# Performance work log

Measured on AMD Instinct MI355X. Metric: run time of the kernel, lower is better.

The kernel has to match this reference:

```python
import jax, jax.numpy as jnp
import numpy as np

N_NODES = 50000
N_EDGES = 800000
NUM_GRAPHS = 256
H = 128          # h_dim
C = H + 1        # CGConv channels = 129
Z = 2 * C + 1    # concat(x_i, x_j, edge_attr) = 259
N_GRAPH_LAYERS = 5
N_FC = 3
OUT_DIM = 1


def setup_inputs() -> dict:
    key = jax.random.key(0)
    ks = jax.random.split(key, 12)
    atoms = jax.random.randint(ks[0], (N_NODES,), 0, 119)
    pos = jax.random.normal(ks[1], (N_NODES, 3), dtype=jnp.float32)
    edge_index = jax.random.randint(ks[2], (2, N_EDGES), 0, N_NODES)
    batch = jnp.sort(jax.random.randint(ks[3], (N_NODES,), 0, NUM_GRAPHS))
    s = 0.05
    emb = jax.random.normal(ks[4], (119, H), dtype=jnp.float32)
    Wf = jax.random.normal(ks[5], (N_GRAPH_LAYERS, Z, C), dtype=jnp.float32) * s
    bf = jnp.zeros((N_GRAPH_LAYERS, C), dtype=jnp.float32)
    Ws = jax.random.normal(ks[6], (N_GRAPH_LAYERS, Z, C), dtype=jnp.float32) * s
    bs = jnp.zeros((N_GRAPH_LAYERS, C), dtype=jnp.float32)
    Wfc = jax.random.normal(ks[7], (N_FC, C, C), dtype=jnp.float32) * s
    bfc = jnp.zeros((N_FC, C), dtype=jnp.float32)
    Wout = jax.random.normal(ks[8], (C, OUT_DIM), dtype=jnp.float32) * s
    bout = jnp.zeros((OUT_DIM,), dtype=jnp.float32)
    return {"atoms": atoms, "pos": pos, "edge_index": edge_index, "batch": batch,
            "emb": emb, "Wf": Wf, "bf": bf, "Ws": Ws, "bs": bs,
            "Wfc": Wfc, "bfc": bfc, "Wout": Wout, "bout": bout}


def reference(atoms, pos, edge_index, batch, emb, Wf, bf, Ws, bs, Wfc, bfc, Wout, bout):
    n = atoms.shape[0]
    src, dst = edge_index[0], edge_index[1]  # PyG: x_j = x[src], x_i = x[dst], aggregate at dst
    # edge_attr = ||pos[src] - pos[dst]||, shape [E, 1]
    edge_attr = jnp.linalg.norm(pos[src] - pos[dst], axis=-1, keepdims=True)
    # node features: atom embedding + z-coordinate -> [N, 129]
    x = jnp.concatenate([emb[atoms], pos[:, 2:3]], axis=-1)
    for l in range(Wf.shape[0]):
        z = jnp.concatenate([x[dst], x[src], edge_attr], axis=-1)  # [E, 259]
        m = jax.nn.sigmoid(z @ Wf[l] + bf[l]) * jax.nn.softplus(z @ Ws[l] + bs[l])
        x = x + jax.ops.segment_sum(m, dst, num_segments=n)  # CGConv: aggr='add' + residual
    # mean pooling per graph
    sums = jax.ops.segment_sum(x, batch, num_segments=NUM_GRAPHS)
    cnts = jax.ops.segment_sum(jnp.ones((n, 1), x.dtype), batch, num_segments=NUM_GRAPHS)
    g = sums / jnp.maximum(cnts, 1.0)
    for l in range(Wfc.shape[0]):
        g = g @ Wfc[l] + bfc[l]
    return g @ Wout + bout
```

## Files before the change

kernel.cpp:

```cpp
#include <hip/hip_runtime.h>
#include <math.h>

#define N_NODES 50000
#define N_EDGES 800000
#define NUM_GRAPHS 256
#define NPADROWS 50048
#define CAP 64
#define SCLN -1.44269504088896f
#define SCLP 1.44269504088896f
#define C693 0.69314718056f
#define LROW 264

typedef __attribute__((ext_vector_type(8))) short short8;
typedef __attribute__((ext_vector_type(4))) float f32x4;
typedef __attribute__((ext_vector_type(2))) float f32x2;

__device__ __forceinline__ float fast_rcp(float x) {
#if __has_builtin(__builtin_amdgcn_rcpf)
  return __builtin_amdgcn_rcpf(x);
#else
  return 1.0f / x;
#endif
}
__device__ __forceinline__ float EX2(float x) {
#if __has_builtin(__builtin_amdgcn_exp2f)
  return __builtin_amdgcn_exp2f(x);
#else
  return exp2f(x);
#endif
}
__device__ __forceinline__ float LG2(float x) {
#if __has_builtin(__builtin_amdgcn_logf)
  return __builtin_amdgcn_logf(x);
#else
  return log2f(x);
#endif
}
__device__ __forceinline__ unsigned f2bf(float x) {
  unsigned u = __float_as_uint(x);
  return (u + 0x7fffu + ((u >> 16) & 1u)) >> 16;
}
__device__ __forceinline__ unsigned short bfr(float v) {
  return (unsigned short)((__float_as_uint(v) + 0x8000u) >> 16);
}
__device__ __forceinline__ unsigned pkbfr(float lo, float hi) {
  unsigned a = (__float_as_uint(lo) + 0x8000u) >> 16;
  unsigned b = (__float_as_uint(hi) + 0x8000u) & 0xffff0000u;
  return a | b;
}
__device__ __forceinline__ float u2f(unsigned u) { return __uint_as_float(u); }
__device__ __forceinline__ f32x2 mk2(float a, float b) {
  f32x2 r; r.x = a; r.y = b; return r;
}
__device__ __forceinline__ f32x2 unp(unsigned u) {
  return mk2(u2f(u << 16), u2f(u & 0xffff0000u));
}
__device__ __forceinline__ f32x2 lg2p1(f32x2 t) {
  f32x2 p = __builtin_elementwise_fma(t, (f32x2)0.0439245f, (f32x2)-0.1898214f);
  p = __builtin_elementwise_fma(t, p, (f32x2)0.4115517f);
  p = __builtin_elementwise_fma(t, p, (f32x2)-0.7072504f);
  p = __builtin_elementwise_fma(t, p, (f32x2)1.4415927f);
  return t * p;
}
__device__ __forceinline__ void edge_ch2(f32x2 gf, f32x2 gs, f32x2& acc) {
  f32x2 den = mk2(EX2(gf.x), EX2(gf.y)) + 1.0f;
  f32x2 ts = mk2(EX2(-fabsf(gs.x)), EX2(-fabsf(gs.y)));
  f32x2 sp = lg2p1(ts) + __builtin_elementwise_max(gs, (f32x2)0.0f);
  f32x2 rc = mk2(fast_rcp(den.x), fast_rcp(den.y));
  acc = __builtin_elementwise_fma(rc, sp, acc);
}

__global__ void init_x(const int* __restrict__ atoms, const float* __restrict__ pos,
                       const float* __restrict__ emb, float* __restrict__ x128c,
                       unsigned* __restrict__ xbu, float4* __restrict__ pos4,
                       int* __restrict__ cnt) {
  int n = blockIdx.x;
  int t = threadIdx.x;
  int a = atoms[n];
  float2 e = *(const float2*)(emb + (size_t)a * 128 + 2 * t);
  xbu[(size_t)n * 64 + t] = f2bf(e.x) | (f2bf(e.y) << 16);
  if (t == 0) x128c[n] = pos[n * 3 + 2];
  if (t == 1) pos4[n] = make_float4(pos[3 * n], pos[3 * n + 1], pos[3 * n + 2], 0.f);
  if (t == 2) cnt[n] = 0;
}

__global__ void prep_b(const float* __restrict__ Wf, const float* __restrict__ Ws,
                       const float* __restrict__ bfp, const float* __restrict__ bsp,
                       uint4* __restrict__ Bp, float2* __restrict__ Wtail) {
  int idx = blockIdx.x * 256 + threadIdx.x;
  if (idx < 5 * 4 * 9 * 4 * 64) {
    int lane = idx & 63;
    int t = idx >> 6;
    int ks = t & 3; t >>= 2;
    int ct = t % 9; t /= 9;
    int g = t & 3;
    int l = t >> 2;
    const float* W = (g >= 2) ? Ws : Wf;
    float sc = (g < 2) ? SCLN : SCLP;
    int col = ct * 16 + (lane & 15);
    int kb = ks * 32 + (lane >> 4) * 8;
    unsigned u[4];
#pragma unroll
    for (int p = 0; p < 4; ++p) {
      unsigned lo = 0, hi = 0;
      if (col < 129) {
        int k0 = kb + 2 * p, k1 = k0 + 1;
        int r0 = (g & 1) ? 129 + k0 : k0;
        int r1 = (g & 1) ? 129 + k1 : k1;
        lo = f2bf(sc * W[(size_t)(l * 259 + r0) * 129 + col]);
        hi = f2bf(sc * W[(size_t)(l * 259 + r1) * 129 + col]);
      }
      u[p] = lo | (hi << 16);
    }
    Bp[idx] = make_uint4(u[0], u[1], u[2], u[3]);
  } else {
    int j = idx - 5 * 4 * 9 * 4 * 64;
    if (j >= 5 * 4 * 144) return;
    int c = j % 144;
    int t = j / 144;
    int g = t & 3;
    int l = t >> 2;
    float sc = (g < 2) ? SCLN : SCLP;
    float w1 = 0.0f, bias = 0.0f;
    if (c <= 128) {
      const float* W = (g >= 2) ? Ws : Wf;
      int row = (g & 1) ? 257 : 128;
      w1 = sc * W[(size_t)(l * 259 + row) * 129 + c];
      if (g == 0) bias = SCLN * bfp[l * 129 + c];
      if (g == 2) bias = SCLP * bsp[l * 129 + c];
    }
    Wtail[(l * 4 + g) * 144 + c] = make_float2(w1, bias);
  }
}

__global__ void build_csr(const int* __restrict__ ei, const float4* __restrict__ pos4,
                          const int* __restrict__ batch, int* __restrict__ cnt,
                          int2* __restrict__ csr, int* __restrict__ goff) {
  int e = blockIdx.x * 256 + threadIdx.x;
  if (e <= N_NODES) {
    int b = (e < N_NODES) ? batch[e] : NUM_GRAPHS;
    int bp = (e > 0) ? batch[e - 1] : -1;
    for (int g = bp + 1; g <= b; ++g) goff[g] = e;
  }
  if (e >= N_EDGES) return;
  int s = ei[e];
  int d = ei[N_EDGES + e];
  float4 ps = pos4[s];
  float4 pd = pos4[d];
  float dx = ps.x - pd.x, dy = ps.y - pd.y, dz = ps.z - pd.z;
  float ea = sqrtf(dx * dx + dy * dy + dz * dz);
  int p = atomicAdd(&cnt[d], 1);
  if (p < CAP) csr[d * CAP + p] = make_int2(s, __float_as_int(ea));
}

__global__ __launch_bounds__(256) void gemm_mfma(
    const unsigned* __restrict__ xbu, const float* __restrict__ x128c,
    const uint4* __restrict__ Bp, const float2* __restrict__ Wtail,
    unsigned short* __restrict__ Pdh, unsigned short* __restrict__ Pfs,
    unsigned* __restrict__ Pd128c, unsigned* __restrict__ Pc128, int layer) {
  __shared__ short smA[32 * 136];
  __shared__ unsigned short ldsD[32 * LROW];
  __shared__ unsigned short ldsS[32 * LROW];
  int n0 = blockIdx.x * 32;
  int tid = threadIdx.x;
  for (int ch = tid; ch < 512; ch += 256) {
    int row = ch >> 4, cq = ch & 15;
    *(uint4*)(&smA[row * 136 + cq * 8]) =
        *(const uint4*)(xbu + (size_t)(n0 + row) * 64 + cq * 4);
  }
  __syncthreads();
  int g = tid >> 6;
  int l = tid & 63;
  int q = l >> 4, c16 = l & 15;
  const short8* Bp8 = (const short8*)Bp;
  int bbase = (layer * 4 + g) * 9 * 4;
  f32x4 acc[2][9];
#pragma unroll
  for (int rt = 0; rt < 2; ++rt)
#pragma unroll
    for (int ct = 0; ct < 9; ++ct) acc[rt][ct] = (f32x4){0.f, 0.f, 0.f, 0.f};
#pragma unroll
  for (int ks = 0; ks < 4; ++ks) {
    short8 a0 = *(const short8*)(&smA[c16 * 136 + (ks * 4 + q) * 8]);
    short8 a1 = *(const short8*)(&smA[(16 + c16) * 136 + (ks * 4 + q) * 8]);
#pragma unroll
    for (int ct = 0; ct < 9; ++ct) {
      short8 b = Bp8[(size_t)(bbase + ct * 4 + ks) * 64 + l];
      acc[0][ct] = __builtin_amdgcn_mfma_f32_16x16x32_bf16(a0, b, acc[0][ct], 0, 0, 0);
      acc[1][ct] = __builtin_amdgcn_mfma_f32_16x16x32_bf16(a1, b, acc[1][ct], 0, 0, 0);
    }
  }
  const float2* Wt = Wtail + (layer * 4 + g) * 144;
  float x128[2][4];
#pragma unroll
  for (int rt = 0; rt < 2; ++rt)
#pragma unroll
    for (int r = 0; r < 4; ++r)
      x128[rt][r] = x128c[n0 + rt * 16 + q * 4 + r];
  unsigned short* ldsO = (g & 1) ? ldsS : ldsD;
  int soff = (g >= 2) ? 2 : 0;
  unsigned short* c128p = (g & 1) ? (unsigned short*)Pc128 : (unsigned short*)Pd128c;
  int c128o = (g >= 2) ? 1 : 0;
#pragma unroll
  for (int ct = 0; ct < 9; ++ct) {
    int col = ct * 16 + c16;
    float2 wb = Wt[col];
#pragma unroll
    for (int rt = 0; rt < 2; ++rt) {
#pragma unroll
      for (int r = 0; r < 4; ++r) {
        int rl = rt * 16 + q * 4 + r;
        float v = acc[rt][ct][r] + fmaf(x128[rt][r], wb.x, wb.y);
        if (col < 128) {
          ldsO[rl * LROW + ((col >> 1) << 2) + soff + (col & 1)] = bfr(v);
        } else if (col == 128) {
          c128p[2 * (size_t)(n0 + rl) + c128o] = bfr(v);
        }
      }
    }
  }
  __syncthreads();
#pragma unroll
  for (int i = tid; i < 2048; i += 256) {
    int img = i >> 10;
    int c = i & 1023;
    int row = c >> 5, part = c & 31;
    const unsigned short* src = (img ? ldsS : ldsD) + row * LROW + part * 8;
    unsigned short* dst = (img ? Pfs : Pdh) + (size_t)(n0 + row) * 256 + part * 8;
    *(uint4*)dst = *(const uint4*)src;
  }
}

__global__ __launch_bounds__(256) void edge_agg(
    const unsigned short* __restrict__ Pdh, const unsigned short* __restrict__ Pfs,
    const unsigned* __restrict__ Pd128c, const unsigned* __restrict__ Pc128,
    unsigned* __restrict__ xbu, float* __restrict__ x128c, const int* __restrict__ cnt,
    const int2* __restrict__ csr, const float* __restrict__ WfL,
    const float* __restrict__ WsL) {
  int lane = threadIdx.x & 63;
  int half = lane >> 5;
  int l5 = lane & 31;
  int n = blockIdx.x * 4 + (threadIdx.x >> 6);
  if (n >= N_NODES) return;
  int nu = __builtin_amdgcn_readfirstlane(n);
  const float* wfl = WfL + 258 * 129;
  const float* wsl = WsL + 258 * 129;
  uint4 pdv = *(const uint4*)(Pdh + (size_t)nu * 256 + 8 * l5);
  f32x2 bfa = unp(pdv.x), bsa = unp(pdv.y), bfb = unp(pdv.z), bsb = unp(pdv.w);
  float2 wfa0 = *(const float2*)(wfl + 4 * l5);
  float2 wfb0 = *(const float2*)(wfl + 4 * l5 + 2);
  float2 wsa0 = *(const float2*)(wsl + 4 * l5);
  float2 wsb0 = *(const float2*)(wsl + 4 * l5 + 2);
  f32x2 wfa = mk2(SCLN * wfa0.x, SCLN * wfa0.y), wfb = mk2(SCLN * wfb0.x, SCLN * wfb0.y);
  f32x2 wsa = mk2(SCLP * wsa0.x, SCLP * wsa0.y), wsb = mk2(SCLP * wsb0.x, SCLP * wsb0.y);
  unsigned pd1 = Pd128c[nu];
  float bfc8 = u2f(pd1 << 16), bsc8 = u2f(pd1 & 0xffff0000u);
  float wfc8 = SCLN * wfl[128], wsc8 = SCLP * wsl[128];
  int m = cnt[nu];
  if (m > CAP) m = CAP;
  const int4* cb4 = (const int4*)(csr + (size_t)nu * CAP);
  const uint4* Pfq = (const uint4*)Pfs;
  f32x2 accA = (f32x2)0.0f, accB = (f32x2)0.0f;

#define GATHER(qq) Pfq[(size_t)(half ? qq.z : qq.x) * 32 + l5]
#define COMPUTE(qq, gg)                                                       \
  {                                                                           \
    f32x2 ea_ = (f32x2)__int_as_float(half ? qq.w : qq.y);                    \
    edge_ch2(__builtin_elementwise_fma(ea_, wfa, bfa + unp(gg.x)),            \
             __builtin_elementwise_fma(ea_, wsa, bsa + unp(gg.y)), accA);     \
    edge_ch2(__builtin_elementwise_fma(ea_, wfb, bfb + unp(gg.z)),            \
             __builtin_elementwise_fma(ea_, wsb, bsb + unp(gg.w)), accB);     \
  }

  int Pf = m >> 1;
  int4 qc = make_int4(0, 0, 0, 0);
  uint4 gc = make_uint4(0, 0, 0, 0);
  if (Pf > 0) {
    qc = cb4[0];
    gc = GATHER(qc);
  }
  for (int p = 0; p < Pf; ++p) {
    int4 qn = qc;
    uint4 gn = gc;
    if (p + 1 < Pf) {
      qn = cb4[p + 1];
      gn = GATHER(qn);
    }
    COMPUTE(qc, gc);
    qc = qn;
    gc = gn;
  }
  if ((m & 1) && half == 0) {
    int4 qt = cb4[Pf];
    f32x2 ea_ = (f32x2)__int_as_float(qt.y);
    uint4 gt = Pfq[(size_t)qt.x * 32 + l5];
    edge_ch2(__builtin_elementwise_fma(ea_, wfa, bfa + unp(gt.x)),
             __builtin_elementwise_fma(ea_, wsa, bsa + unp(gt.y)), accA);
    edge_ch2(__builtin_elementwise_fma(ea_, wfb, bfb + unp(gt.z)),
             __builtin_elementwise_fma(ea_, wsb, bsb + unp(gt.w)), accB);
  }
#undef GATHER
#undef COMPUTE

  accA.x += __shfl_xor(accA.x, 32, 64);
  accA.y += __shfl_xor(accA.y, 32, 64);
  accB.x += __shfl_xor(accB.x, 32, 64);
  accB.y += __shfl_xor(accB.y, 32, 64);

  float v2 = 0.f;
  if (lane < m) {
    int2 se = csr[(size_t)nu * CAP + lane];
    float ea = __int_as_float(se.y);
    unsigned pc = Pc128[se.x];
    float f2 = u2f(pc << 16), s2 = u2f(pc & 0xffff0000u);
    float gf2 = fmaf(ea, wfc8, bfc8 + f2);
    float gs2 = fmaf(ea, wsc8, bsc8 + s2);
    float sp2 = LG2(1.0f + EX2(-fabsf(gs2))) + fmaxf(gs2, 0.0f);
    v2 = C693 * fast_rcp(1.0f + EX2(gf2)) * sp2;
  }
#pragma unroll
  for (int off = 32; off; off >>= 1) v2 += __shfl_down(v2, off, 64);

  if (half == 0) {
    uint2 xv = *(const uint2*)(xbu + (size_t)nu * 64 + 2 * l5);
    f32x2 xa = __builtin_elementwise_fma(accA, (f32x2)C693, unp(xv.x));
    f32x2 xb = __builtin_elementwise_fma(accB, (f32x2)C693, unp(xv.y));
    *(uint2*)(xbu + (size_t)nu * 64 + 2 * l5) =
        make_uint2(pkbfr(xa.x, xa.y), pkbfr(xb.x, xb.y));
  }
  if (lane == 0) x128c[nu] += v2;
}

__global__ void pool2(const unsigned* __restrict__ xbu, const float* __restrict__ x128c,
                      const int* __restrict__ goff, float* __restrict__ gpart) {
  int gph = blockIdx.x >> 2;
  int q = blockIdx.x & 3;
  int t = threadIdx.x;
  if (t >= 129) return;
  int s = goff[gph], e = goff[gph + 1];
  int len = e - s;
  int chunk = (len + 3) >> 2;
  int a = s + q * chunk;
  int b = a + chunk; if (b > e) b = e;
  float acc = 0.f;
  if (t < 128) {
    int w = t >> 1, hi = t & 1;
    for (int n = a; n < b; ++n) {
      unsigned u = xbu[(size_t)n * 64 + w];
      acc += hi ? u2f(u & 0xffff0000u) : u2f(u << 16);
    }
  } else {
    for (int n = a; n < b; ++n) acc += x128c[n];
  }
  gpart[(size_t)(gph * 4 + q) * 132 + t] = acc;
}

__global__ void fcout(const float* __restrict__ gpart, const int* __restrict__ goff,
                      const float* __restrict__ Wfc, const float* __restrict__ bfc,
                      const float* __restrict__ Wout, const float* __restrict__ bout,
                      float* __restrict__ out) {
  __shared__ float buf[2][132];
  __shared__ float red[3];
  int i = blockIdx.x;
  int t = threadIdx.x;
  bool act = t < 129;
  int len = goff[i + 1] - goff[i];
  float inv = fast_rcp(fmaxf((float)len, 1.0f));
  if (act) {
    float v = gpart[(size_t)(i * 4 + 0) * 132 + t] + gpart[(size_t)(i * 4 + 1) * 132 + t] +
              gpart[(size_t)(i * 4 + 2) * 132 + t] + gpart[(size_t)(i * 4 + 3) * 132 + t];
    buf[0][t] = v * inv;
  }
  __syncthreads();
  int cur = 0;
#pragma unroll
  for (int l = 0; l < 3; ++l) {
    float s = 0.f;
    if (act) {
      const float* Wl = Wfc + (size_t)l * 129 * 129 + t;
      s = bfc[l * 129 + t];
      float wA[16], wB[16];
      float wlast = Wl[(size_t)128 * 129];
#pragma unroll
      for (int j = 0; j < 16; ++j) wA[j] = Wl[(size_t)j * 129];
#pragma unroll
      for (int kb = 0; kb < 128; kb += 16) {
        const int gidx = kb >> 4;
        float* wc = (gidx & 1) ? wB : wA;
        float* wn = (gidx & 1) ? wA : wB;
        if (kb + 16 < 128) {
#pragma unroll
          for (int j = 0; j < 16; ++j) wn[j] = Wl[(size_t)(kb + 16 + j) * 129];
        }
#pragma unroll
        for (int j = 0; j < 16; ++j) s = fmaf(buf[cur][kb + j], wc[j], s);
      }
      s = fmaf(buf[cur][128], wlast, s);
    }
    __syncthreads();
    if (act) buf[1 - cur][t] = s;
    cur = 1 - cur;
    __syncthreads();
  }
  float p = act ? buf[cur][t] * Wout[t] : 0.f;
#pragma unroll
  for (int off = 32; off; off >>= 1) p += __shfl_down(p, off, 64);
  if ((t & 63) == 0) red[t >> 6] = p;
  __syncthreads();
  if (t == 0) out[i] = red[0] + red[1] + red[2] + bout[0];
}

extern "C" void kernel_launch(void* const* d_in, const int* in_sizes, int n_in,
                              void* d_out, int out_size, void* d_ws, size_t ws_size,
                              hipStream_t stream) {
  const int* atoms = (const int*)d_in[0];
  const float* pos = (const float*)d_in[1];
  const int* ei = (const int*)d_in[2];
  const int* batch = (const int*)d_in[3];
  const float* emb = (const float*)d_in[4];
  const float* Wf = (const float*)d_in[5];
  const float* bfp = (const float*)d_in[6];
  const float* Ws = (const float*)d_in[7];
  const float* bsp = (const float*)d_in[8];
  const float* Wfc = (const float*)d_in[9];
  const float* bfc = (const float*)d_in[10];
  const float* Wout = (const float*)d_in[11];
  const float* bout = (const float*)d_in[12];
  float* outp = (float*)d_out;

  uint4* Bp = (uint4*)d_ws;
  unsigned* xbu = (unsigned*)(Bp + 46080);
  unsigned short* Pdh = (unsigned short*)(xbu + (size_t)NPADROWS * 64);
  unsigned short* Pfs = Pdh + (size_t)NPADROWS * 256;
  float4* pos4 = (float4*)(Pfs + (size_t)NPADROWS * 256);
  float2* Wtail = (float2*)(pos4 + N_NODES);
  float* x128c = (float*)(Wtail + 5 * 4 * 144);
  float* gpart = x128c + NPADROWS;
  int* goff = (int*)(gpart + 256 * 4 * 132);
  int* cnt = goff + 260;
  int2* csr = (int2*)(cnt + N_NODES + 4);
  unsigned* Pd128c = (unsigned*)(csr + (size_t)N_NODES * CAP);
  unsigned* Pc128 = Pd128c + NPADROWS;

  init_x<<<N_NODES, 64, 0, stream>>>(atoms, pos, emb, x128c, xbu, pos4, cnt);
  prep_b<<<(5 * 4 * 9 * 4 * 64 + 5 * 4 * 144 + 255) / 256, 256, 0, stream>>>(
      Wf, Ws, bfp, bsp, Bp, Wtail);
  build_csr<<<(N_EDGES + 255) / 256, 256, 0, stream>>>(ei, pos4, batch, cnt, csr, goff);

  for (int l = 0; l < 5; ++l) {
    gemm_mfma<<<NPADROWS / 32, 256, 0, stream>>>(xbu, x128c, Bp, Wtail, Pdh, Pfs,
                                                 Pd128c, Pc128, l);
    edge_agg<<<(N_NODES + 3) / 4, 256, 0, stream>>>(Pdh, Pfs, Pd128c, Pc128, xbu, x128c,
                                                    cnt, csr,
                                                    Wf + (size_t)l * 259 * 129,
                                                    Ws + (size_t)l * 259 * 129);
  }

  pool2<<<NUM_GRAPHS * 4, 192, 0, stream>>>(xbu, x128c, goff, gpart);
  fcout<<<NUM_GRAPHS, 192, 0, stream>>>(gpart, goff, Wfc, bfc, Wout, bout, outp);
}
```

Measured before the change: 635.1 us.

## Swap MFMA operands, prefetch B fragments, store GEMM outputs directly without LDS staging

Swaps the A/B operands of the MFMA so each lane holds four consecutive output channels for one node. The epilogue can then pack pairs into 32-bit bf16 writes straight to global memory, removing the LDS output buffers, one barrier and the copy-out loop. It also loads the B fragments one k-step ahead in registers and overlaps the x tile global load with the first B loads. The cost is higher register pressure and narrower, strided global stores in place of coalesced 16-byte writes.

After: 718.9 us. 13.2% more time.

```diff
diff --git a/kernel.cpp b/kernel.cpp
--- a/kernel.cpp
+++ b/kernel.cpp
@@ -9,7 +9,6 @@
 #define SCLN -1.44269504088896f
 #define SCLP 1.44269504088896f
 #define C693 0.69314718056f
-#define LROW 264
 
 typedef __attribute__((ext_vector_type(8))) short short8;
 typedef __attribute__((ext_vector_type(4))) float f32x4;
@@ -159,75 +158,77 @@
     unsigned short* __restrict__ Pdh, unsigned short* __restrict__ Pfs,
     unsigned* __restrict__ Pd128c, unsigned* __restrict__ Pc128, int layer) {
   __shared__ short smA[32 * 136];
-  __shared__ unsigned short ldsD[32 * LROW];
-  __shared__ unsigned short ldsS[32 * LROW];
   int n0 = blockIdx.x * 32;
   int tid = threadIdx.x;
-  for (int ch = tid; ch < 512; ch += 256) {
-    int row = ch >> 4, cq = ch & 15;
-    *(uint4*)(&smA[row * 136 + cq * 8]) =
-        *(const uint4*)(xbu + (size_t)(n0 + row) * 64 + cq * 4);
-  }
-  __syncthreads();
   int g = tid >> 6;
   int l = tid & 63;
   int q = l >> 4, c16 = l & 15;
   const short8* Bp8 = (const short8*)Bp;
-  int bbase = (layer * 4 + g) * 9 * 4;
+  const short8* Bq = Bp8 + (size_t)((layer * 4 + g) * 9 * 4) * 64 + l;
+
+  int row0 = tid >> 4, cq = tid & 15;
+  uint4 st0 = *(const uint4*)(xbu + (size_t)(n0 + row0) * 64 + cq * 4);
+  uint4 st1 = *(const uint4*)(xbu + (size_t)(n0 + 16 + row0) * 64 + cq * 4);
+  short8 b[9];
+#pragma unroll
+  for (int ct = 0; ct < 9; ++ct) b[ct] = Bq[(size_t)(ct * 4) * 64];
+  *(uint4*)(&smA[row0 * 136 + cq * 8]) = st0;
+  *(uint4*)(&smA[(16 + row0) * 136 + cq * 8]) = st1;
+  __syncthreads();
+
   f32x4 acc[2][9];
 #pragma unroll
-  for (int rt = 0; rt < 2; ++rt)
-#pragma unroll
-    for (int ct = 0; ct < 9; ++ct) acc[rt][ct] = (f32x4){0.f, 0.f, 0.f, 0.f};
+  for (int nt = 0; nt < 2; ++nt)
+#pragma unroll
+    for (int ct = 0; ct < 9; ++ct) acc[nt][ct] = (f32x4){0.f, 0.f, 0.f, 0.f};
 #pragma unroll
   for (int ks = 0; ks < 4; ++ks) {
     short8 a0 = *(const short8*)(&smA[c16 * 136 + (ks * 4 + q) * 8]);
     short8 a1 = *(const short8*)(&smA[(16 + c16) * 136 + (ks * 4 + q) * 8]);
+    short8 bn[9];
+    if (ks < 3) {
+#pragma unroll
+      for (int ct = 0; ct < 9; ++ct) bn[ct] = Bq[(size_t)(ct * 4 + ks + 1) * 64];
+    }
 #pragma unroll
     for (int ct = 0; ct < 9; ++ct) {
-      short8 b = Bp8[(size_t)(bbase + ct * 4 + ks) * 64 + l];
-      acc[0][ct] = __builtin_amdgcn_mfma_f32_16x16x32_bf16(a0, b, acc[0][ct], 0, 0, 0);
-      acc[1][ct] = __builtin_amdgcn_mfma_f32_16x16x32_bf16(a1, b, acc[1][ct], 0, 0, 0);
-    }
-  }
-  const float2* Wt = Wtail + (layer * 4 + g) * 144;
-  float x128[2][4];
-#pragma unroll
-  for (int rt = 0; rt < 2; ++rt)
-#pragma unroll
-    for (int r = 0; r < 4; ++r)
-      x128[rt][r] = x128c[n0 + rt * 16 + q * 4 + r];
-  unsigned short* ldsO = (g & 1) ? ldsS : ldsD;
-  int soff = (g >= 2) ? 2 : 0;
+      acc[0][ct] = __builtin_amdgcn_mfma_f32_16x16x32_bf16(b[ct], a0, acc[0][ct], 0, 0, 0);
+      acc[1][ct] = __builtin_amdgcn_mfma_f32_16x16x32_bf16(b[ct], a1, acc[1][ct], 0, 0, 0);
+    }
+    if (ks < 3) {
+#pragma unroll
+      for (int ct = 0; ct < 9; ++ct) b[ct] = bn[ct];
+    }
+  }
+
+  const float4* Wt4 = (const float4*)(Wtail + (layer * 4 + g) * 144);
+  float xv[2];
+  xv[0] = x128c[n0 + c16];
+  xv[1] = x128c[n0 + 16 + c16];
+  unsigned* P32 = (unsigned*)((g & 1) ? Pfs : Pdh);
+  int sof = (g >= 2) ? 1 : 0;
   unsigned short* c128p = (g & 1) ? (unsigned short*)Pc128 : (unsigned short*)Pd128c;
   int c128o = (g >= 2) ? 1 : 0;
 #pragma unroll
   for (int ct = 0; ct < 9; ++ct) {
-    int col = ct * 16 + c16;
-    float2 wb = Wt[col];
-#pragma unroll
-    for (int rt = 0; rt < 2; ++rt) {
-#pragma unroll
-      for (int r = 0; r < 4; ++r) {
-        int rl = rt * 16 + q * 4 + r;
-        float v = acc[rt][ct][r] + fmaf(x128[rt][r], wb.x, wb.y);
-        if (col < 128) {
-          ldsO[rl * LROW + ((col >> 1) << 2) + soff + (col & 1)] = bfr(v);
-        } else if (col == 128) {
-          c128p[2 * (size_t)(n0 + rl) + c128o] = bfr(v);
-        }
+    int ch0 = ct * 16 + 4 * q;
+    float4 wba = Wt4[ch0 >> 1];
+    float4 wbb = Wt4[(ch0 >> 1) + 1];
+#pragma unroll
+    for (int nt = 0; nt < 2; ++nt) {
+      int node = n0 + nt * 16 + c16;
+      float v0 = acc[nt][ct][0] + fmaf(xv[nt], wba.x, wba.y);
+      float v1 = acc[nt][ct][1] + fmaf(xv[nt], wba.z, wba.w);
+      float v2 = acc[nt][ct][2] + fmaf(xv[nt], wbb.x, wbb.y);
+      float v3 = acc[nt][ct][3] + fmaf(xv[nt], wbb.z, wbb.w);
+      if (ct < 8) {
+        unsigned* dst = P32 + (size_t)node * 128 + ch0 + sof;
+        dst[0] = pkbfr(v0, v1);
+        dst[2] = pkbfr(v2, v3);
+      } else if (q == 0) {
+        c128p[2 * (size_t)node + c128o] = bfr(v0);
       }
     }
-  }
-  __syncthreads();
-#pragma unroll
-  for (int i = tid; i < 2048; i += 256) {
-    int img = i >> 10;
-    int c = i & 1023;
-    int row = c >> 5, part = c & 31;
-    const unsigned short* src = (img ? ldsS : ldsD) + row * LROW + part * 8;
-    unsigned short* dst = (img ? Pfs : Pdh) + (size_t)(n0 + row) * 256 + part * 8;
-    *(uint4*)dst = *(const uint4*)src;
   }
 }
 
```
